# Kernel optimization log

Hardware: AMD Instinct MI355X
Metric: run time of the kernel (lower is better)

The kernel has to match this reference:

```python
import jax, jax.numpy as jnp
import numpy as np

N = 100000   # total nodes across the ragged graph batch
E = 800000   # edges
B = 4096     # graphs
V = 103      # element vocab (embedding rows)
D_IN = 200   # embedding dim
H = 256      # hidden dim


def setup_inputs() -> dict:
    key = jax.random.key(0)
    ks = jax.random.split(key, 20)
    s = 0.05
    return {
        "weight": jax.random.normal(ks[0], (V, D_IN), jnp.float32),
        "sto_x": jax.random.randint(ks[1], (N,), 0, V),
        "sto_edge_index": jax.random.randint(ks[2], (2, E), 0, N),
        "sto_weight": jax.random.uniform(ks[3], (N,), jnp.float32),
        "sto_batch": jnp.sort(jax.random.randint(ks[4], (N,), 0, B)),
        "gW0": jax.random.normal(ks[5], (D_IN, H), jnp.float32) * s,
        "gb0": jnp.zeros((H,), jnp.float32),
        "gW1": jax.random.normal(ks[6], (H, H), jnp.float32) * s,
        "gb1": jnp.zeros((H,), jnp.float32),
        "gW2": jax.random.normal(ks[7], (H, H), jnp.float32) * s,
        "gb2": jnp.zeros((H,), jnp.float32),
        "lstm_Wih": jax.random.normal(ks[8], (4 * H, 2 * H), jnp.float32) * s,
        "lstm_Whh": jax.random.normal(ks[9], (4 * H, H), jnp.float32) * s,
        "lstm_bih": jnp.zeros((4 * H,), jnp.float32),
        "lstm_bhh": jnp.zeros((4 * H,), jnp.float32),
        "mlin_W": jax.random.normal(ks[10], (H, 2 * H), jnp.float32) * s,
        "mlin_b": jnp.zeros((H,), jnp.float32),
        "p0W": jax.random.normal(ks[11], (128, H), jnp.float32) * s,
        "p0b": jnp.zeros((128,), jnp.float32),
        "p1W": jax.random.normal(ks[12], (128, 128), jnp.float32) * s,
        "p1b": jnp.zeros((128,), jnp.float32),
        "p2W": jax.random.normal(ks[13], (1, 128), jnp.float32) * s,
        "p2b": jnp.zeros((1,), jnp.float32),
    }


def reference(weight, sto_x, sto_edge_index, sto_weight, sto_batch,
              gW0, gb0, gW1, gb1, gW2, gb2,
              lstm_Wih, lstm_Whh, lstm_bih, lstm_bhh,
              mlin_W, mlin_b, p0W, p0b, p1W, p1b, p2W, p2b):
    # embedding gather (sto_x - 1, with -1 wrapping to the last row as in torch)
    x = weight[sto_x - 1]

    # --- GCN (3 layers, symmetric norm with self-loops, ReLU between layers) ---
    loop = jnp.arange(N)
    src = jnp.concatenate([sto_edge_index[0], loop])
    dst = jnp.concatenate([sto_edge_index[1], loop])
    deg = jax.ops.segment_sum(jnp.ones_like(dst, jnp.float32), dst, N)
    dinv = jax.lax.rsqrt(jnp.maximum(deg, 1.0))
    norm = (dinv[src] * dinv[dst])[:, None]

    def conv(h_in, W, b):
        hw = h_in @ W                                   # [N, H]
        return jax.ops.segment_sum(hw[src] * norm, dst, N) + b

    x = jax.nn.relu(conv(x, gW0, gb0))
    x = jax.nn.relu(conv(x, gW1, gb1))
    x = conv(x, gW2, gb2)

    # --- stoichiometric weighting + graph-wise scatter sum ---
    wx = x * sto_weight[:, None]                        # [N, H]
    sto = jax.ops.segment_sum(wx, sto_batch, B)         # [B, H]

    # --- Set2Set pooling (2 processing steps, 1-layer LSTM) ---
    h = jnp.zeros((B, H), wx.dtype)
    c = jnp.zeros((B, H), wx.dtype)
    q_star = jnp.zeros((B, 2 * H), wx.dtype)
    for _ in range(2):
        gates = q_star @ lstm_Wih.T + lstm_bih + h @ lstm_Whh.T + lstm_bhh
        i, f, g, o = jnp.split(gates, 4, axis=-1)
        c = jax.nn.sigmoid(f) * c + jax.nn.sigmoid(i) * jnp.tanh(g)
        h = jax.nn.sigmoid(o) * jnp.tanh(c)
        e = jnp.sum(wx * h[sto_batch], axis=-1)         # [N]
        emax = jax.ops.segment_max(e, sto_batch, B)
        a = jnp.exp(e - emax[sto_batch])
        a = a / (jax.ops.segment_sum(a, sto_batch, B)[sto_batch] + 1e-16)
        r = jax.ops.segment_sum(wx * a[:, None], sto_batch, B)
        q_star = jnp.concatenate([h, r], axis=-1)

    mean = q_star @ mlin_W.T + mlin_b + sto
    mean = mean / jnp.maximum(jnp.linalg.norm(mean, axis=1, keepdims=True), 1e-12)

    # --- predictor MLP (LeakyReLU slope 0.01) ---
    y = jax.nn.leaky_relu(mean @ p0W.T + p0b)
    y = jax.nn.leaky_relu(y @ p1W.T + p1b)
    return y @ p2W.T + p2b                              # [B, 1]
```

## Files before the change

kernel.cpp:

```cpp
#include <hip/hip_runtime.h>
#include <math.h>

constexpr int Nn  = 100000;
constexpr int Ee  = 800000;
constexpr int Bb  = 4096;
constexpr int Vv  = 103;
constexpr int DIN = 200;
constexpr int Hh  = 256;
constexpr int KV  = 128;

constexpr int SCHUNK = 1024;
constexpr int NSCAN  = (Nn + SCHUNK - 1)/SCHUNK;

using short8 = __attribute__((ext_vector_type(8))) short;
using f32x4  = __attribute__((ext_vector_type(4))) float;

__device__ __forceinline__ float sigf(float x){ return 1.f/(1.f+expf(-x)); }

__device__ __forceinline__ unsigned short f2bf(float f){
  unsigned int u = __float_as_uint(f);
  u += 0x7FFFu + ((u >> 16) & 1u);
  return (unsigned short)(u >> 16);
}
__device__ __forceinline__ float bf2f(unsigned int u){
  return __uint_as_float((u & 0xFFFFu) << 16);
}

__global__ void k_transpose(const float* __restrict__ in, float* __restrict__ out, int R, int C){
  int idx = blockIdx.x*256 + threadIdx.x;
  if (idx >= R*C) return;
  int r = idx / C, c = idx % C;
  out[(size_t)c*R + r] = in[(size_t)r*C + c];
}

__global__ void k_transpose_b(const float* __restrict__ in, unsigned short* __restrict__ out, int R, int C){
  int idx = blockIdx.x*256 + threadIdx.x;
  if (idx >= R*C) return;
  int r = idx / C, c = idx % C;
  out[(size_t)c*R + r] = f2bf(in[(size_t)r*C + c]);
}

__global__ void k_castb(const float* __restrict__ in, unsigned short* __restrict__ out, int n){
  int i = blockIdx.x*256 + threadIdx.x;
  if (i < n) out[i] = f2bf(in[i]);
}

__global__ void k_wg0t(const float* __restrict__ WG0, unsigned short* __restrict__ WG0tb){
  int i = blockIdx.x*256 + threadIdx.x;
  if (i >= Hh*KV) return;
  int n = i >> 7, k = i & (KV-1);
  float v = (k < Vv) ? WG0[(size_t)k*Hh + n] : 0.f;
  WG0tb[i] = f2bf(v);
}

__global__ void k_packW(const float* __restrict__ Wih, const float* __restrict__ Whh,
                        unsigned short* __restrict__ Wp){
  int i = blockIdx.x*256 + threadIdx.x;
  if (i >= 4*Hh*3*Hh) return;
  int g = i / (3*Hh), j = i % (3*Hh);
  float v = (j < 2*Hh) ? Wih[(size_t)g*2*Hh + j] : Whh[(size_t)g*Hh + (j - 2*Hh)];
  Wp[i] = f2bf(v);
}

__global__ void k_count(const int* __restrict__ dst, int* __restrict__ counts){
  int e = blockIdx.x*256 + threadIdx.x;
  if (e < Ee) atomicAdd(&counts[dst[e]], 1);
}

__global__ void k_dinv(const int* __restrict__ counts, float* __restrict__ dinv){
  int n = blockIdx.x*256 + threadIdx.x;
  if (n < Nn) dinv[n] = rsqrtf((float)(counts[n] + 1));
}

__global__ void k_scan1(const int* __restrict__ counts, int* __restrict__ partial){
  __shared__ int red[256];
  int t = threadIdx.x;
  int base = blockIdx.x*SCHUNK + t*4;
  int s = 0;
  if (base + 3 < Nn){ int4 v = *reinterpret_cast<const int4*>(counts + base); s = v.x+v.y+v.z+v.w; }
  else { for (int i=0;i<4;++i) if (base+i<Nn) s += counts[base+i]; }
  red[t] = s; __syncthreads();
  for (int st=128; st>0; st>>=1){ if (t<st) red[t]+=red[t+st]; __syncthreads(); }
  if (t==0) partial[blockIdx.x] = red[0];
}

__global__ void k_scan2(int* __restrict__ partial, int n){
  __shared__ int buf[128];
  int t = threadIdx.x;
  int v = (t < n) ? partial[t] : 0;
  buf[t] = v; __syncthreads();
  for (int off=1; off<128; off<<=1){
    int tv = (t>=off) ? buf[t-off] : 0;
    __syncthreads();
    buf[t] += tv;
    __syncthreads();
  }
  if (t < n) partial[t] = buf[t] - v;
}

__global__ void k_scan3(const int* __restrict__ counts, const int* __restrict__ partial,
                        int* __restrict__ offs){
  __shared__ int red[256];
  int t = threadIdx.x;
  int base = blockIdx.x*SCHUNK + t*4;
  int c0=0,c1=0,c2=0,c3=0;
  if (base + 3 < Nn){ int4 v = *reinterpret_cast<const int4*>(counts + base); c0=v.x;c1=v.y;c2=v.z;c3=v.w; }
  else { if (base<Nn) c0=counts[base]; if (base+1<Nn) c1=counts[base+1];
         if (base+2<Nn) c2=counts[base+2]; if (base+3<Nn) c3=counts[base+3]; }
  int s = c0+c1+c2+c3;
  red[t] = s; __syncthreads();
  for (int off=1; off<256; off<<=1){
    int tv = (t>=off) ? red[t-off] : 0;
    __syncthreads();
    red[t] += tv;
    __syncthreads();
  }
  int run = partial[blockIdx.x] + red[t] - s;
  if (base   < Nn) offs[base]   = run; run += c0;
  if (base+1 < Nn) offs[base+1] = run; run += c1;
  if (base+2 < Nn) offs[base+2] = run; run += c2;
  if (base+3 < Nn) offs[base+3] = run; run += c3;
  if (blockIdx.x == gridDim.x-1 && t == 255) offs[Nn] = partial[blockIdx.x] + red[255];
}

__global__ void k_copyi(const int* __restrict__ a, int* __restrict__ b, int n){
  int i = blockIdx.x*256 + threadIdx.x;
  if (i < n) b[i] = a[i];
}

__global__ void k_fill(const int* __restrict__ ei, const float* __restrict__ dinv,
                       int* __restrict__ fptr, uint2* __restrict__ epack){
  int e = blockIdx.x*256 + threadIdx.x;
  if (e >= Ee) return;
  int s = ei[e], d = ei[Ee + e];
  int pos = atomicAdd(&fptr[d], 1);
  epack[pos] = make_uint2((unsigned int)s, __float_as_uint(dinv[s]*dinv[d]));
}

__global__ void k_boffs(const int* __restrict__ batch, int* __restrict__ boffs){
  int b = blockIdx.x*256 + threadIdx.x;
  if (b > Bb) return;
  int lo = 0, hi = Nn;
  while (lo < hi){ int mid = (lo+hi)>>1; if (batch[mid] < b) lo = mid+1; else hi = mid; }
  boffs[b] = lo;
}

__global__ void k_hist(const int* __restrict__ sto_x, const int* __restrict__ offs,
                       const uint2* __restrict__ epack, const float* __restrict__ dinv,
                       unsigned short* __restrict__ Vb){
  __shared__ float hist[4][KV];
  int wid = threadIdx.x >> 6, lane = threadIdx.x & 63;
  int n = blockIdx.x*4 + wid;
  hist[wid][lane] = 0.f; hist[wid][lane+64] = 0.f;
  __syncthreads();
  int s = offs[n], e = offs[n+1];
  for (int k = s + lane; k < e; k += 64){
    uint2 ev = epack[k];
    int r2 = sto_x[ev.x]; r2 = (r2 == 0) ? (Vv-1) : r2-1;
    atomicAdd(&hist[wid][r2], __uint_as_float(ev.y));
  }
  if (lane == 0){
    int r0 = sto_x[n]; r0 = (r0 == 0) ? (Vv-1) : r0-1;
    float dn = dinv[n];
    atomicAdd(&hist[wid][r0], dn*dn);
  }
  __syncthreads();
  unsigned int p = ((unsigned int)f2bf(hist[wid][2*lane+1]) << 16) | f2bf(hist[wid][2*lane]);
  ((unsigned int*)Vb)[(size_t)n*(KV/2) + lane] = p;
}

__global__ void k_agg(const unsigned short* __restrict__ Xb, const int* __restrict__ offs,
                      const uint2* __restrict__ epack, const float* __restrict__ dinv,
                      unsigned short* __restrict__ T){
  int wid = threadIdx.x >> 6, lane = threadIdx.x & 63;
  int n = blockIdx.x*4 + wid;
  const uint2* Xv = (const uint2*)Xb;
  uint2 v = Xv[(size_t)n*64 + lane];
  float dn = dinv[n]; float s2 = dn*dn;
  float a0 = bf2f(v.x)*s2, a1 = bf2f(v.x>>16)*s2;
  float a2 = bf2f(v.y)*s2, a3 = bf2f(v.y>>16)*s2;
  int s = offs[n], e = offs[n+1];
  int k = s;
  for (; k + 7 < e; k += 8){
    uint2 ev[8], g[8];
    #pragma unroll
    for (int j = 0; j < 8; ++j) ev[j] = epack[k+j];
    #pragma unroll
    for (int j = 0; j < 8; ++j) g[j] = Xv[(size_t)ev[j].x*64 + lane];
    #pragma unroll
    for (int j = 0; j < 8; ++j){
      float nn = __uint_as_float(ev[j].y);
      a0 += bf2f(g[j].x)*nn; a1 += bf2f(g[j].x>>16)*nn;
      a2 += bf2f(g[j].y)*nn; a3 += bf2f(g[j].y>>16)*nn;
    }
  }
  for (; k + 1 < e; k += 2){
    uint2 e0 = epack[k], e1 = epack[k+1];
    uint2 g0 = Xv[(size_t)e0.x*64 + lane];
    uint2 g1 = Xv[(size_t)e1.x*64 + lane];
    float n0 = __uint_as_float(e0.y), n1 = __uint_as_float(e1.y);
    a0 += bf2f(g0.x)*n0; a1 += bf2f(g0.x>>16)*n0; a2 += bf2f(g0.y)*n0; a3 += bf2f(g0.y>>16)*n0;
    a0 += bf2f(g1.x)*n1; a1 += bf2f(g1.x>>16)*n1; a2 += bf2f(g1.y)*n1; a3 += bf2f(g1.y>>16)*n1;
  }
  if (k < e){
    uint2 e0 = epack[k];
    uint2 g0 = Xv[(size_t)e0.x*64 + lane];
    float n0 = __uint_as_float(e0.y);
    a0 += bf2f(g0.x)*n0; a1 += bf2f(g0.x>>16)*n0;
    a2 += bf2f(g0.y)*n0; a3 += bf2f(g0.y>>16)*n0;
  }
  uint2 o;
  o.x = (unsigned int)f2bf(a0) | ((unsigned int)f2bf(a1) << 16);
  o.y = (unsigned int)f2bf(a2) | ((unsigned int)f2bf(a3) << 16);
  ((uint2*)T)[(size_t)n*64 + lane] = o;
}

__global__ __launch_bounds__(512) void k_gemm64(
    const unsigned short* __restrict__ A, int lda,
    const unsigned short* __restrict__ Bt,
    const float* __restrict__ bias, const float* __restrict__ rowscale,
    const float* __restrict__ addf,
    float* __restrict__ Cf, unsigned short* __restrict__ Cb,
    int M, int K, int Nc, int relu)
{
  __shared__ unsigned short lds[23040];
  unsigned short (*Al)[72] = (unsigned short(*)[72])lds;
  unsigned short (*Bl)[72] = (unsigned short(*)[72])(lds + 64*72);

  int tid = threadIdx.x;
  int w = tid >> 6, lane = tid & 63;
  int wr = (w >> 2)*32, wc = (w & 3)*64;
  int l16 = lane & 15, kh = lane >> 4;
  int rbase = blockIdx.y*64, cbase = blockIdx.x*256;
  int sr = tid >> 3, sb = tid & 7;

  f32x4 acc[2][4] = {};

  for (int k0 = 0; k0 < K; k0 += 64){
    int kk = k0 + sb*8;
    uint4 a0 = make_uint4(0,0,0,0);
    int ar = rbase + sr;
    if (ar < M) a0 = *reinterpret_cast<const uint4*>(A + (size_t)ar*lda + kk);
    uint4 b0 = *reinterpret_cast<const uint4*>(Bt + (size_t)(cbase + sr      )*K + kk);
    uint4 b1 = *reinterpret_cast<const uint4*>(Bt + (size_t)(cbase + sr +  64)*K + kk);
    uint4 b2 = *reinterpret_cast<const uint4*>(Bt + (size_t)(cbase + sr + 128)*K + kk);
    uint4 b3 = *reinterpret_cast<const uint4*>(Bt + (size_t)(cbase + sr + 192)*K + kk);
    __syncthreads();
    *reinterpret_cast<uint4*>(&Al[sr][sb*8])     = a0;
    *reinterpret_cast<uint4*>(&Bl[sr][sb*8])     = b0;
    *reinterpret_cast<uint4*>(&Bl[sr+64][sb*8])  = b1;
    *reinterpret_cast<uint4*>(&Bl[sr+128][sb*8]) = b2;
    *reinterpret_cast<uint4*>(&Bl[sr+192][sb*8]) = b3;
    __syncthreads();

    #pragma unroll
    for (int kq = 0; kq < 2; ++kq){
      short8 af[2], bfv[4];
      #pragma unroll
      for (int m = 0; m < 2; ++m)
        af[m] = *reinterpret_cast<const short8*>(&Al[wr + m*16 + l16][kq*32 + kh*8]);
      #pragma unroll
      for (int n2 = 0; n2 < 4; ++n2)
        bfv[n2] = *reinterpret_cast<const short8*>(&Bl[wc + n2*16 + l16][kq*32 + kh*8]);
      #pragma unroll
      for (int m = 0; m < 2; ++m)
        #pragma unroll
        for (int n2 = 0; n2 < 4; ++n2)
          acc[m][n2] = __builtin_amdgcn_mfma_f32_16x16x32_bf16(af[m], bfv[n2], acc[m][n2], 0, 0, 0);
    }
  }

  if (Cf){
    #pragma unroll
    for (int n2 = 0; n2 < 4; ++n2){
      int col = cbase + wc + n2*16 + l16;
      float bv = bias ? bias[col] : 0.f;
      #pragma unroll
      for (int m = 0; m < 2; ++m){
        #pragma unroll
        for (int i = 0; i < 4; ++i){
          int row = rbase + wr + m*16 + kh*4 + i;
          if (row >= M) continue;
          float v = acc[m][n2][i] + bv;
          if (addf) v += addf[(size_t)row*Nc + col];
          if (rowscale) v *= rowscale[row];
          if (relu == 1) v = fmaxf(v, 0.f);
          else if (relu == 2) v = (v > 0.f) ? v : 0.01f*v;
          Cf[(size_t)row*Nc + col] = v;
        }
      }
    }
  }
  if (Cb){
    __syncthreads();
    unsigned short* eps = lds + w*(32*72);
    #pragma unroll
    for (int n2 = 0; n2 < 4; ++n2){
      int colg = cbase + wc + n2*16 + l16;
      float bv = bias ? bias[colg] : 0.f;
      #pragma unroll
      for (int m = 0; m < 2; ++m){
        #pragma unroll
        for (int i = 0; i < 4; ++i){
          int lrow = m*16 + kh*4 + i;
          int rowg = rbase + wr + lrow;
          float v = acc[m][n2][i] + bv;
          float rs = (rowscale && rowg < M) ? rowscale[rowg] : 1.f;
          v *= rs;
          if (relu == 1) v = fmaxf(v, 0.f);
          else if (relu == 2) v = (v > 0.f) ? v : 0.01f*v;
          eps[lrow*72 + n2*16 + l16] = f2bf(v);
        }
      }
    }
    int c8 = lane & 7;
    #pragma unroll
    for (int rd = 0; rd < 4; ++rd){
      int lrow = rd*8 + (lane >> 3);
      int rowg = rbase + wr + lrow;
      short8 vv = *reinterpret_cast<const short8*>(&eps[lrow*72 + c8*8]);
      if (rowg < M)
        *reinterpret_cast<short8*>(Cb + (size_t)rowg*Nc + cbase + wc + c8*8) = vv;
    }
  }
}

__global__ __launch_bounds__(512) void k_gemm8(
    const unsigned short* __restrict__ A, int lda,
    const unsigned short* __restrict__ Bt,
    const float* __restrict__ bias, const float* __restrict__ rowscale,
    const float* __restrict__ addf,
    float* __restrict__ Cf, unsigned short* __restrict__ Cb,
    int M, int K, int Nc, int relu)
{
  __shared__ unsigned short lds[18432];
  unsigned short (*Al)[40] = (unsigned short(*)[40])lds;
  unsigned short (*Bl)[40] = (unsigned short(*)[40])(lds + 128*40);

  int tid = threadIdx.x;
  int w = tid >> 6, lane = tid & 63;
  int wr = (w >> 1)*32, wc = (w & 1)*64;
  int l16 = lane & 15, kh = lane >> 4;
  int rbase = blockIdx.y*128, cbase = blockIdx.x*128;
  int sr = tid >> 2, sb = tid & 3;

  f32x4 acc[2][4] = {};

  for (int k0 = 0; k0 < K; k0 += 32){
    int kk = k0 + sb*8;
    uint4 a0 = make_uint4(0,0,0,0);
    int ar0 = rbase + sr;
    if (ar0 < M) a0 = *reinterpret_cast<const uint4*>(A + (size_t)ar0*lda + kk);
    uint4 b0 = *reinterpret_cast<const uint4*>(Bt + (size_t)(cbase + sr)*K + kk);
    __syncthreads();
    *reinterpret_cast<uint4*>(&Al[sr][sb*8]) = a0;
    *reinterpret_cast<uint4*>(&Bl[sr][sb*8]) = b0;
    __syncthreads();

    short8 af[2], bfv[4];
    #pragma unroll
    for (int m = 0; m < 2; ++m) af[m] = *reinterpret_cast<const short8*>(&Al[wr + m*16 + l16][kh*8]);
    #pragma unroll
    for (int n2 = 0; n2 < 4; ++n2) bfv[n2] = *reinterpret_cast<const short8*>(&Bl[wc + n2*16 + l16][kh*8]);
    #pragma unroll
    for (int m = 0; m < 2; ++m)
      #pragma unroll
      for (int n2 = 0; n2 < 4; ++n2)
        acc[m][n2] = __builtin_amdgcn_mfma_f32_16x16x32_bf16(af[m], bfv[n2], acc[m][n2], 0, 0, 0);
  }

  if (Cf){
    #pragma unroll
    for (int n2 = 0; n2 < 4; ++n2){
      int col = cbase + wc + n2*16 + l16;
      float bv = bias ? bias[col] : 0.f;
      #pragma unroll
      for (int m = 0; m < 2; ++m){
        #pragma unroll
        for (int i = 0; i < 4; ++i){
          int row = rbase + wr + m*16 + kh*4 + i;
          if (row >= M) continue;
          float v = acc[m][n2][i] + bv;
          if (addf) v += addf[(size_t)row*Nc + col];
          if (rowscale) v *= rowscale[row];
          if (relu == 1) v = fmaxf(v, 0.f);
          else if (relu == 2) v = (v > 0.f) ? v : 0.01f*v;
          Cf[(size_t)row*Nc + col] = v;
        }
      }
    }
  }
  if (Cb){
    __syncthreads();
    unsigned short* eps = lds + w*(32*72);
    #pragma unroll
    for (int n2 = 0; n2 < 4; ++n2){
      int colg = cbase + wc + n2*16 + l16;
      float bv = bias ? bias[colg] : 0.f;
      #pragma unroll
      for (int m = 0; m < 2; ++m){
        #pragma unroll
        for (int i = 0; i < 4; ++i){
          int lrow = m*16 + kh*4 + i;
          int rowg = rbase + wr + lrow;
          float v = acc[m][n2][i] + bv;
          float rs = (rowscale && rowg < M) ? rowscale[rowg] : 1.f;
          v *= rs;
          if (relu == 1) v = fmaxf(v, 0.f);
          else if (relu == 2) v = (v > 0.f) ? v : 0.01f*v;
          eps[lrow*72 + n2*16 + l16] = f2bf(v);
        }
      }
    }
    int c8 = lane & 7;
    #pragma unroll
    for (int rd = 0; rd < 4; ++rd){
      int lrow = rd*8 + (lane >> 3);
      int rowg = rbase + wr + lrow;
      short8 vv = *reinterpret_cast<const short8*>(&eps[lrow*72 + c8*8]);
      if (rowg < M)
        *reinterpret_cast<short8*>(Cb + (size_t)rowg*Nc + cbase + wc + c8*8) = vv;
    }
  }
}

__global__ __launch_bounds__(256) void k_gemm_nt(
    const float* __restrict__ A, const float* __restrict__ Bt,
    const float* __restrict__ bias, const float* __restrict__ Dadd,
    float* __restrict__ C, int M, int K, int Nc, int accum, int act)
{
  __shared__ float As[64][20];
  __shared__ float Bs[64][20];
  int tid = threadIdx.x;
  int rbase = blockIdx.y*64, cbase = blockIdx.x*64;
  int ty = tid>>4, tx = tid&15;
  int lr = tid>>2, lq = tid&3;
  float acc[4][4] = {};
  for (int k0 = 0; k0 < K; k0 += 16){
    float4 av = make_float4(0,0,0,0), bv = make_float4(0,0,0,0);
    int kk = k0 + lq*4;
    int ar = rbase + lr;
    if (ar < M && kk < K){
      if (kk + 3 < K) av = *reinterpret_cast<const float4*>(A + (size_t)ar*K + kk);
      else { float t0[4] = {0,0,0,0}; for (int i=0; i<4 && kk+i<K; ++i) t0[i] = A[(size_t)ar*K + kk + i];
             av = make_float4(t0[0],t0[1],t0[2],t0[3]); }
    }
    int br = cbase + lr;
    if (br < Nc && kk < K){
      if (kk + 3 < K) bv = *reinterpret_cast<const float4*>(Bt + (size_t)br*K + kk);
      else { float t0[4] = {0,0,0,0}; for (int i=0; i<4 && kk+i<K; ++i) t0[i] = Bt[(size_t)br*K + kk + i];
             bv = make_float4(t0[0],t0[1],t0[2],t0[3]); }
    }
    __syncthreads();
    *reinterpret_cast<float4*>(&As[lr][lq*4]) = av;
    *reinterpret_cast<float4*>(&Bs[lr][lq*4]) = bv;
    __syncthreads();
    #pragma unroll
    for (int kc = 0; kc < 16; kc += 4){
      float4 a4[4], b4[4];
      #pragma unroll
      for (int i=0;i<4;++i) a4[i] = *reinterpret_cast<float4*>(&As[ty*4+i][kc]);
      #pragma unroll
      for (int j=0;j<4;++j) b4[j] = *reinterpret_cast<float4*>(&Bs[tx*4+j][kc]);
      #pragma unroll
      for (int i=0;i<4;++i)
        #pragma unroll
        for (int j=0;j<4;++j)
          acc[i][j] += a4[i].x*b4[j].x + a4[i].y*b4[j].y + a4[i].z*b4[j].z + a4[i].w*b4[j].w;
    }
  }
  #pragma unroll
  for (int i=0;i<4;++i){
    int r = rbase + ty*4 + i;
    if (r >= M) continue;
    #pragma unroll
    for (int j=0;j<4;++j){
      int cc = cbase + tx*4 + j;
      if (cc >= Nc) continue;
      float v = acc[i][j];
      if (accum) v += C[(size_t)r*Nc + cc];
      if (bias)  v += bias[cc];
      if (Dadd)  v += Dadd[(size_t)r*Nc + cc];
      if (act == 1) v = (v > 0.f) ? v : 0.01f*v;
      C[(size_t)r*Nc + cc] = v;
    }
  }
}

__global__ void k_bsum(const float* __restrict__ bih, const float* __restrict__ bhh,
                       float* __restrict__ bsum){
  int g = blockIdx.x*256 + threadIdx.x;
  if (g < 4*Hh) bsum[g] = bih[g] + bhh[g];
}

__global__ void k_lstm(const float* __restrict__ gates, float* __restrict__ cbuf,
                       float* __restrict__ hbuf, unsigned short* __restrict__ qh){
  int idx = blockIdx.x*256 + threadIdx.x;
  if (idx >= Bb*Hh) return;
  int b = idx >> 8, ch = idx & 255;
  const float* g = gates + (size_t)b*4*Hh;
  float ig = sigf(g[ch]);
  float fg = sigf(g[Hh + ch]);
  float gg = tanhf(g[2*Hh + ch]);
  float og = sigf(g[3*Hh + ch]);
  float cn = fg*cbuf[idx] + ig*gg;
  float hn = og*tanhf(cn);
  cbuf[idx] = cn; hbuf[idx] = hn;
  unsigned short hb = f2bf(hn);
  qh[(size_t)b*3*Hh + ch] = hb;
  qh[(size_t)b*3*Hh + 2*Hh + ch] = hb;
}

__global__ void k_pool(const unsigned short* __restrict__ wxb,
                       const float* __restrict__ hbuf,
                       const int* __restrict__ boffs,
                       unsigned short* __restrict__ qh,
                       float* __restrict__ sto, int do_sto){
  int wid = threadIdx.x >> 6, lane = threadIdx.x & 63;
  int g = blockIdx.x*4 + wid;
  if (g >= Bb) return;
  const uint2* Xv = (const uint2*)wxb;
  float4 hv = ((const float4*)hbuf)[(size_t)g*64 + lane];
  int s = boffs[g], e = boffs[g+1];
  float m = -INFINITY, ssum = 0.f;
  float a0=0.f,a1=0.f,a2=0.f,a3=0.f;
  float t0=0.f,t1=0.f,t2=0.f,t3=0.f;
  for (int n = s; n < e; ++n){
    uint2 v = Xv[(size_t)n*64 + lane];
    float x0=bf2f(v.x), x1=bf2f(v.x>>16), x2=bf2f(v.y), x3=bf2f(v.y>>16);
    if (do_sto){ t0+=x0; t1+=x1; t2+=x2; t3+=x3; }
    float d = x0*hv.x + x1*hv.y + x2*hv.z + x3*hv.w;
    #pragma unroll
    for (int mask=32; mask; mask>>=1) d += __shfl_xor(d, mask, 64);
    if (d > m){
      float sc = expf(m - d);
      ssum = ssum*sc + 1.f;
      a0 = a0*sc + x0; a1 = a1*sc + x1; a2 = a2*sc + x2; a3 = a3*sc + x3;
      m = d;
    } else {
      float p = expf(d - m);
      ssum += p;
      a0 += p*x0; a1 += p*x1; a2 += p*x2; a3 += p*x3;
    }
  }
  float inv = 1.f/(ssum + 1e-16f);
  uint2 o;
  o.x = (unsigned int)f2bf(a0*inv) | ((unsigned int)f2bf(a1*inv) << 16);
  o.y = (unsigned int)f2bf(a2*inv) | ((unsigned int)f2bf(a3*inv) << 16);
  ((uint2*)(qh + (size_t)g*3*Hh + Hh))[lane] = o;
  if (do_sto) ((float4*)sto)[(size_t)g*64 + lane] = make_float4(t0,t1,t2,t3);
}

__global__ void k_norm(float* __restrict__ mean, unsigned short* __restrict__ outb){
  __shared__ float red[256];
  int b = blockIdx.x, tid = threadIdx.x;
  float v = mean[(size_t)b*Hh + tid];
  red[tid] = v*v; __syncthreads();
  for (int st=128; st>0; st>>=1){ if (tid<st) red[tid] += red[tid+st]; __syncthreads(); }
  float nrm = fmaxf(sqrtf(red[0]), 1e-12f);
  float o = v/nrm;
  outb[(size_t)b*Hh + tid] = f2bf(o);
}

__global__ void k_out(const float* __restrict__ y1, const float* __restrict__ p2W,
                      const float* __restrict__ p2b, float* __restrict__ out){
  __shared__ float red[128];
  int b = blockIdx.x, tid = threadIdx.x;
  float v = y1[(size_t)b*128 + tid]*p2W[tid];
  red[tid] = v; __syncthreads();
  for (int st=64; st>0; st>>=1){ if (tid<st) red[tid] += red[tid+st]; __syncthreads(); }
  if (tid == 0) out[b] = red[0] + p2b[0];
}

extern "C" void kernel_launch(void* const* d_in, const int* in_sizes, int n_in,
                              void* d_out, int out_size, void* d_ws, size_t ws_size,
                              hipStream_t stream) {
  const float* weight   = (const float*)d_in[0];
  const int*   sto_x    = (const int*)  d_in[1];
  const int*   ei       = (const int*)  d_in[2];
  const float* sto_w    = (const float*)d_in[3];
  const int*   batch    = (const int*)  d_in[4];
  const float* gW0 = (const float*)d_in[5];   const float* gb0 = (const float*)d_in[6];
  const float* gW1 = (const float*)d_in[7];   const float* gb1 = (const float*)d_in[8];
  const float* gW2 = (const float*)d_in[9];   const float* gb2 = (const float*)d_in[10];
  const float* Wih = (const float*)d_in[11];  const float* Whh = (const float*)d_in[12];
  const float* bih = (const float*)d_in[13];  const float* bhh = (const float*)d_in[14];
  const float* mW  = (const float*)d_in[15];  const float* mb  = (const float*)d_in[16];
  const float* p0W = (const float*)d_in[17];  const float* p0b = (const float*)d_in[18];
  const float* p1W = (const float*)d_in[19];  const float* p1b = (const float*)d_in[20];
  const float* p2W = (const float*)d_in[21];  const float* p2b = (const float*)d_in[22];
  float* out = (float*)d_out;

  char* w = (char*)d_ws;
  auto alloc = [&](size_t bytes)->char*{ char* p = w; w += (bytes + 255) & ~size_t(255); return p; };
  unsigned short* Xb = (unsigned short*)alloc((size_t)Nn*Hh*2);
  unsigned short* Tb = (unsigned short*)alloc((size_t)Nn*Hh*2);
  unsigned short* Vb = (unsigned short*)alloc((size_t)Nn*KV*2);
  float* WG0   = (float*)alloc((size_t)Vv*Hh*4);
  unsigned short* WG0tb = (unsigned short*)alloc((size_t)Hh*KV*2);
  float* gW0t  = (float*)alloc((size_t)Hh*DIN*4);
  unsigned short* gW1tb = (unsigned short*)alloc((size_t)Hh*Hh*2);
  unsigned short* gW2tb = (unsigned short*)alloc((size_t)Hh*Hh*2);
  unsigned short* Wpb   = (unsigned short*)alloc((size_t)4*Hh*3*Hh*2);
  unsigned short* mWb   = (unsigned short*)alloc((size_t)Hh*2*Hh*2);
  unsigned short* p0Wb  = (unsigned short*)alloc((size_t)128*Hh*2);
  unsigned short* p1Wb  = (unsigned short*)alloc((size_t)128*128*2);
  int*   counts= (int*)  alloc((size_t)Nn*4);
  int*   offs  = (int*)  alloc((size_t)(Nn+1)*4);
  int*   fptr  = (int*)  alloc((size_t)Nn*4);
  int*   spart = (int*)  alloc((size_t)NSCAN*4);
  float* dinv  = (float*)alloc((size_t)Nn*4);
  uint2* epack = (uint2*)alloc((size_t)Ee*8);
  int*   boffs = (int*)  alloc((size_t)(Bb+1)*4);
  float* sto   = (float*)alloc((size_t)Bb*Hh*4);
  float* hbuf  = (float*)alloc((size_t)Bb*Hh*4);
  float* cbuf  = (float*)alloc((size_t)Bb*Hh*4);
  unsigned short* qh = (unsigned short*)alloc((size_t)Bb*3*Hh*2);
  float* gates = (float*)alloc((size_t)Bb*4*Hh*4);
  float* bsum  = (float*)alloc((size_t)4*Hh*4);
  float* meanb = (float*)alloc((size_t)Bb*Hh*4);
  unsigned short* meanbb = (unsigned short*)alloc((size_t)Bb*Hh*2);
  unsigned short* y0b = (unsigned short*)alloc((size_t)Bb*128*2);
  float* y1    = (float*)alloc((size_t)Bb*128*4);

  auto gemm = [&](const float* A, const float* Bt, const float* bias, const float* Dadd,
                  float* C, int M, int K, int Nc, int accum, int act){
    dim3 g((Nc+63)/64, (M+63)/64);
    k_gemm_nt<<<g, 256, 0, stream>>>(A, Bt, bias, Dadd, C, M, K, Nc, accum, act);
  };
  auto gemm8 = [&](const unsigned short* A, int lda, const unsigned short* Bt,
                   const float* bias, const float* rowscale, const float* addf,
                   float* Cf, unsigned short* Cb, int M, int K, int Nc, int relu){
    dim3 g(Nc/128, (M+127)/128);
    k_gemm8<<<g, 512, 0, stream>>>(A, lda, Bt, bias, rowscale, addf, Cf, Cb, M, K, Nc, relu);
  };
  auto gemm64 = [&](const unsigned short* A, int lda, const unsigned short* Bt,
                    const float* bias, const float* rowscale, const float* addf,
                    float* Cf, unsigned short* Cb, int M, int K, int Nc, int relu){
    dim3 g(Nc/256, (M+63)/64);
    k_gemm64<<<g, 512, 0, stream>>>(A, lda, Bt, bias, rowscale, addf, Cf, Cb, M, K, Nc, relu);
  };

  hipMemsetAsync(counts, 0, (size_t)Nn*4, stream);
  hipMemsetAsync(cbuf,  0, (size_t)Bb*Hh*4, stream);
  hipMemsetAsync(qh,    0, (size_t)Bb*3*Hh*2, stream);

  k_transpose<<<(DIN*Hh+255)/256, 256, 0, stream>>>(gW0, gW0t, DIN, Hh);
  k_transpose_b<<<(Hh*Hh+255)/256, 256, 0, stream>>>(gW1, gW1tb, Hh, Hh);
  k_transpose_b<<<(Hh*Hh+255)/256, 256, 0, stream>>>(gW2, gW2tb, Hh, Hh);
  k_packW<<<(4*Hh*3*Hh+255)/256, 256, 0, stream>>>(Wih, Whh, Wpb);
  k_castb<<<(Hh*2*Hh+255)/256, 256, 0, stream>>>(mW, mWb, Hh*2*Hh);
  k_castb<<<(128*Hh+255)/256, 256, 0, stream>>>(p0W, p0Wb, 128*Hh);
  k_castb<<<(128*128+255)/256, 256, 0, stream>>>(p1W, p1Wb, 128*128);

  k_count<<<(Ee+255)/256, 256, 0, stream>>>(ei + Ee, counts);
  k_dinv<<<(Nn+255)/256, 256, 0, stream>>>(counts, dinv);
  k_scan1<<<NSCAN, 256, 0, stream>>>(counts, spart);
  k_scan2<<<1, 128, 0, stream>>>(spart, NSCAN);
  k_scan3<<<NSCAN, 256, 0, stream>>>(counts, spart, offs);
  k_copyi<<<(Nn+255)/256, 256, 0, stream>>>(offs, fptr, Nn);
  k_fill<<<(Ee+255)/256, 256, 0, stream>>>(ei, dinv, fptr, epack);
  k_boffs<<<(Bb+256)/256, 256, 0, stream>>>(batch, boffs);

  gemm(weight, gW0t, nullptr, nullptr, WG0, Vv, DIN, Hh, 0, 0);
  k_wg0t<<<(Hh*KV+255)/256, 256, 0, stream>>>(WG0, WG0tb);
  k_hist<<<Nn/4, 256, 0, stream>>>(sto_x, offs, epack, dinv, Vb);
  gemm64(Vb, KV, WG0tb, gb0, nullptr, nullptr, nullptr, Xb, Nn, KV, Hh, 1);

  k_agg<<<Nn/4, 256, 0, stream>>>(Xb, offs, epack, dinv, Tb);
  gemm64(Tb, Hh, gW1tb, gb1, nullptr, nullptr, nullptr, Xb, Nn, Hh, Hh, 1);
  k_agg<<<Nn/4, 256, 0, stream>>>(Xb, offs, epack, dinv, Tb);
  gemm64(Tb, Hh, gW2tb, gb2, sto_w, nullptr, nullptr, Xb, Nn, Hh, Hh, 0);

  k_bsum<<<(4*Hh+255)/256, 256, 0, stream>>>(bih, bhh, bsum);

  for (int t = 0; t < 2; ++t){
    gemm64(qh, 3*Hh, Wpb, bsum, nullptr, nullptr, gates, nullptr, Bb, 3*Hh, 4*Hh, 0);
    k_lstm<<<(Bb*Hh+255)/256, 256, 0, stream>>>(gates, cbuf, hbuf, qh);
    k_pool<<<Bb/4, 256, 0, stream>>>(Xb, hbuf, boffs, qh, sto, t == 0);
  }

  gemm64(qh, 3*Hh, mWb, mb, nullptr, sto, meanb, nullptr, Bb, 2*Hh, Hh, 0);
  k_norm<<<Bb, Hh, 0, stream>>>(meanb, meanbb);
  gemm8(meanbb, Hh, p0Wb, p0b, nullptr, nullptr, nullptr, y0b, Bb, Hh, 128, 2);
  gemm8(y0b, 128, p1Wb, p1b, nullptr, nullptr, y1, nullptr, Bb, 128, 128, 2);
  k_out<<<Bb, 128, 0, stream>>>(y1, p2W, p2b, out);
}
```

Before: 560.3 us.

## Replace histogram+GEMM first GCN layer with direct gather of projected embeddings

The first GCN layer previously built a per-node 128-bin vocabulary histogram and then ran a dense N×128×256 GEMM. It now gathers bf16 rows of the precomputed weight@W0 table per edge (using a per-edge byte vocab index written during CSR fill) and applies bias and ReLU directly. Separately, many small prep kernels (transposes, casts, batch offsets, bias sum, dinv, copy) are merged into one prep kernel or folded into the scan kernels to cut launch count. The trade is more gather traffic per edge in exchange for removing the histogram atomics, the intermediate Vb buffer and one large GEMM.

Result: no change. 551.0 us (-1.7%).

```diff
diff --git a/kernel.cpp b/kernel.cpp
--- a/kernel.cpp
+++ b/kernel.cpp
@@ -7,7 +7,6 @@
 constexpr int Vv  = 103;
 constexpr int DIN = 200;
 constexpr int Hh  = 256;
-constexpr int KV  = 128;
 
 constexpr int SCHUNK = 1024;
 constexpr int NSCAN  = (Nn + SCHUNK - 1)/SCHUNK;
@@ -26,40 +25,70 @@
   return __uint_as_float((u & 0xFFFFu) << 16);
 }
 
-__global__ void k_transpose(const float* __restrict__ in, float* __restrict__ out, int R, int C){
+constexpr int PW_A = DIN*Hh;
+constexpr int PW_B = Hh*Hh;
+constexpr int PW_C = Hh*Hh;
+constexpr int PW_D = 4*Hh*3*Hh;
+constexpr int PW_E = Hh*2*Hh;
+constexpr int PW_F = 128*Hh;
+constexpr int PW_G = 128*128;
+constexpr int PW_H = Bb + 1;
+constexpr int PW_I = 4*Hh;
+constexpr int PW_TOT = PW_A+PW_B+PW_C+PW_D+PW_E+PW_F+PW_G+PW_H+PW_I;
+
+__global__ void k_prep(const float* __restrict__ gW0, float* __restrict__ gW0t,
+                       const float* __restrict__ gW1, unsigned short* __restrict__ gW1tb,
+                       const float* __restrict__ gW2, unsigned short* __restrict__ gW2tb,
+                       const float* __restrict__ Wih, const float* __restrict__ Whh,
+                       unsigned short* __restrict__ Wpb,
+                       const float* __restrict__ mW, unsigned short* __restrict__ mWb,
+                       const float* __restrict__ p0W, unsigned short* __restrict__ p0Wb,
+                       const float* __restrict__ p1W, unsigned short* __restrict__ p1Wb,
+                       const int* __restrict__ batch, int* __restrict__ boffs,
+                       const float* __restrict__ bih, const float* __restrict__ bhh,
+                       float* __restrict__ bsum){
   int idx = blockIdx.x*256 + threadIdx.x;
-  if (idx >= R*C) return;
-  int r = idx / C, c = idx % C;
-  out[(size_t)c*R + r] = in[(size_t)r*C + c];
-}
-
-__global__ void k_transpose_b(const float* __restrict__ in, unsigned short* __restrict__ out, int R, int C){
-  int idx = blockIdx.x*256 + threadIdx.x;
-  if (idx >= R*C) return;
-  int r = idx / C, c = idx % C;
-  out[(size_t)c*R + r] = f2bf(in[(size_t)r*C + c]);
-}
-
-__global__ void k_castb(const float* __restrict__ in, unsigned short* __restrict__ out, int n){
-  int i = blockIdx.x*256 + threadIdx.x;
-  if (i < n) out[i] = f2bf(in[i]);
-}
-
-__global__ void k_wg0t(const float* __restrict__ WG0, unsigned short* __restrict__ WG0tb){
-  int i = blockIdx.x*256 + threadIdx.x;
-  if (i >= Hh*KV) return;
-  int n = i >> 7, k = i & (KV-1);
-  float v = (k < Vv) ? WG0[(size_t)k*Hh + n] : 0.f;
-  WG0tb[i] = f2bf(v);
-}
-
-__global__ void k_packW(const float* __restrict__ Wih, const float* __restrict__ Whh,
-                        unsigned short* __restrict__ Wp){
-  int i = blockIdx.x*256 + threadIdx.x;
-  if (i >= 4*Hh*3*Hh) return;
-  int g = i / (3*Hh), j = i % (3*Hh);
-  float v = (j < 2*Hh) ? Wih[(size_t)g*2*Hh + j] : Whh[(size_t)g*Hh + (j - 2*Hh)];
-  Wp[i] = f2bf(v);
+  if (idx >= PW_TOT) return;
+  if (idx < PW_A){
+    int r = idx / Hh, c = idx % Hh;
+    gW0t[(size_t)c*DIN + r] = gW0[idx];
+    return;
+  }
+  idx -= PW_A;
+  if (idx < PW_B){
+    int r = idx >> 8, c = idx & 255;
+    gW1tb[(size_t)c*Hh + r] = f2bf(gW1[idx]);
+    return;
+  }
+  idx -= PW_B;
+  if (idx < PW_C){
+    int r = idx >> 8, c = idx & 255;
+    gW2tb[(size_t)c*Hh + r] = f2bf(gW2[idx]);
+    return;
+  }
+  idx -= PW_C;
+  if (idx < PW_D){
+    int g = idx / (3*Hh), j = idx % (3*Hh);
+    float v = (j < 2*Hh) ? Wih[(size_t)g*2*Hh + j] : Whh[(size_t)g*Hh + (j - 2*Hh)];
+    Wpb[idx] = f2bf(v);
+    return;
+  }
+  idx -= PW_D;
+  if (idx < PW_E){ mWb[idx] = f2bf(mW[idx]); return; }
+  idx -= PW_E;
+  if (idx < PW_F){ p0Wb[idx] = f2bf(p0W[idx]); return; }
+  idx -= PW_F;
+  if (idx < PW_G){ p1Wb[idx] = f2bf(p1W[idx]); return; }
+  idx -= PW_G;
+  if (idx < PW_H){
+    int b = idx;
+    int lo = 0, hi = Nn;
+    while (lo < hi){ int mid = (lo+hi)>>1; if (batch[mid] < b) lo = mid+1; else hi = mid; }
+    boffs[b] = lo;
+    return;
+  }
+  idx -= PW_H;
+  bsum[idx] = bih[idx] + bhh[idx];
 }
 
 __global__ void k_count(const int* __restrict__ dst, int* __restrict__ counts){
@@ -67,18 +96,22 @@
   if (e < Ee) atomicAdd(&counts[dst[e]], 1);
 }
 
-__global__ void k_dinv(const int* __restrict__ counts, float* __restrict__ dinv){
-  int n = blockIdx.x*256 + threadIdx.x;
-  if (n < Nn) dinv[n] = rsqrtf((float)(counts[n] + 1));
-}
-
-__global__ void k_scan1(const int* __restrict__ counts, int* __restrict__ partial){
+__global__ void k_scan1(const int* __restrict__ counts, int* __restrict__ partial,
+                        float* __restrict__ dinv){
   __shared__ int red[256];
   int t = threadIdx.x;
   int base = blockIdx.x*SCHUNK + t*4;
   int s = 0;
-  if (base + 3 < Nn){ int4 v = *reinterpret_cast<const int4*>(counts + base); s = v.x+v.y+v.z+v.w; }
-  else { for (int i=0;i<4;++i) if (base+i<Nn) s += counts[base+i]; }
+  if (base + 3 < Nn){
+    int4 v = *reinterpret_cast<const int4*>(counts + base);
+    s = v.x+v.y+v.z+v.w;
+    dinv[base]   = rsqrtf((float)(v.x + 1));
+    dinv[base+1] = rsqrtf((float)(v.y + 1));
+    dinv[base+2] = rsqrtf((float)(v.z + 1));
+    dinv[base+3] = rsqrtf((float)(v.w + 1));
+  } else {
+    for (int i=0;i<4;++i) if (base+i<Nn){ int c = counts[base+i]; s += c; dinv[base+i] = rsqrtf((float)(c+1)); }
+  }
   red[t] = s; __syncthreads();
   for (int st=128; st>0; st>>=1){ if (t<st) red[t]+=red[t+st]; __syncthreads(); }
   if (t==0) partial[blockIdx.x] = red[0];
@@ -99,7 +132,7 @@
 }
 
 __global__ void k_scan3(const int* __restrict__ counts, const int* __restrict__ partial,
-                        int* __restrict__ offs){
+                        int* __restrict__ offs, int* __restrict__ fptr){
   __shared__ int red[256];
   int t = threadIdx.x;
   int base = blockIdx.x*SCHUNK + t*4;
@@ -116,57 +149,66 @@
     __syncthreads();
   }
   int run = partial[blockIdx.x] + red[t] - s;
-  if (base   < Nn) offs[base]   = run; run += c0;
-  if (base+1 < Nn) offs[base+1] = run; run += c1;
-  if (base+2 < Nn) offs[base+2] = run; run += c2;
-  if (base+3 < Nn) offs[base+3] = run; run += c3;
+  if (base   < Nn){ offs[base]   = run; fptr[base]   = run; } run += c0;
+  if (base+1 < Nn){ offs[base+1] = run; fptr[base+1] = run; } run += c1;
+  if (base+2 < Nn){ offs[base+2] = run; fptr[base+2] = run; } run += c2;
+  if (base+3 < Nn){ offs[base+3] = run; fptr[base+3] = run; } run += c3;
   if (blockIdx.x == gridDim.x-1 && t == 255) offs[Nn] = partial[blockIdx.x] + red[255];
 }
 
-__global__ void k_copyi(const int* __restrict__ a, int* __restrict__ b, int n){
-  int i = blockIdx.x*256 + threadIdx.x;
-  if (i < n) b[i] = a[i];
-}
-
 __global__ void k_fill(const int* __restrict__ ei, const float* __restrict__ dinv,
-                       int* __restrict__ fptr, uint2* __restrict__ epack){
+                       const int* __restrict__ sto_x, int* __restrict__ fptr,
+                       uint2* __restrict__ epack, unsigned char* __restrict__ evoc){
   int e = blockIdx.x*256 + threadIdx.x;
   if (e >= Ee) return;
   int s = ei[e], d = ei[Ee + e];
   int pos = atomicAdd(&fptr[d], 1);
   epack[pos] = make_uint2((unsigned int)s, __float_as_uint(dinv[s]*dinv[d]));
-}
-
-__global__ void k_boffs(const int* __restrict__ batch, int* __restrict__ boffs){
-  int b = blockIdx.x*256 + threadIdx.x;
-  if (b > Bb) return;
-  int lo = 0, hi = Nn;
-  while (lo < hi){ int mid = (lo+hi)>>1; if (batch[mid] < b) lo = mid+1; else hi = mid; }
-  boffs[b] = lo;
-}
-
-__global__ void k_hist(const int* __restrict__ sto_x, const int* __restrict__ offs,
-                       const uint2* __restrict__ epack, const float* __restrict__ dinv,
-                       unsigned short* __restrict__ Vb){
-  __shared__ float hist[4][KV];
+  int v = sto_x[s];
+  evoc[pos] = (unsigned char)((v == 0) ? (Vv-1) : v-1);
+}
+
+__global__ void k_conv0(const unsigned short* __restrict__ WG0b, const int* __restrict__ sto_x,
+                        const int* __restrict__ offs, const uint2* __restrict__ epack,
+                        const unsigned char* __restrict__ evoc, const float* __restrict__ dinv,
+                        const float* __restrict__ bias, unsigned short* __restrict__ Xb){
   int wid = threadIdx.x >> 6, lane = threadIdx.x & 63;
   int n = blockIdx.x*4 + wid;
-  hist[wid][lane] = 0.f; hist[wid][lane+64] = 0.f;
-  __syncthreads();
+  const uint2* Wv = (const uint2*)WG0b;
+  int v0 = sto_x[n]; int r0 = (v0 == 0) ? (Vv-1) : v0-1;
+  float dn = dinv[n]; float s2 = dn*dn;
+  uint2 w0 = Wv[(size_t)r0*64 + lane];
+  float a0 = bf2f(w0.x)*s2, a1 = bf2f(w0.x>>16)*s2;
+  float a2 = bf2f(w0.y)*s2, a3 = bf2f(w0.y>>16)*s2;
   int s = offs[n], e = offs[n+1];
-  for (int k = s + lane; k < e; k += 64){
+  int k = s;
+  for (; k + 7 < e; k += 8){
+    uint2 ev[8]; int rv[8]; uint2 g[8];
+    #pragma unroll
+    for (int j = 0; j < 8; ++j){ ev[j] = epack[k+j]; rv[j] = evoc[k+j]; }
+    #pragma unroll
+    for (int j = 0; j < 8; ++j) g[j] = Wv[(size_t)rv[j]*64 + lane];
+    #pragma unroll
+    for (int j = 0; j < 8; ++j){
+      float nn = __uint_as_float(ev[j].y);
+      a0 += bf2f(g[j].x)*nn; a1 += bf2f(g[j].x>>16)*nn;
+      a2 += bf2f(g[j].y)*nn; a3 += bf2f(g[j].y>>16)*nn;
+    }
+  }
+  for (; k < e; ++k){
     uint2 ev = epack[k];
-    int r2 = sto_x[ev.x]; r2 = (r2 == 0) ? (Vv-1) : r2-1;
-    atomicAdd(&hist[wid][r2], __uint_as_float(ev.y));
-  }
-  if (lane == 0){
-    int r0 = sto_x[n]; r0 = (r0 == 0) ? (Vv-1) : r0-1;
-    float dn = dinv[n];
-    atomicAdd(&hist[wid][r0], dn*dn);
-  }
-  __syncthreads();
-  unsigned int p = ((unsigned int)f2bf(hist[wid][2*lane+1]) << 16) | f2bf(hist[wid][2*lane]);
-  ((unsigned int*)Vb)[(size_t)n*(KV/2) + lane] = p;
+    uint2 g = Wv[(size_t)evoc[k]*64 + lane];
+    float nn = __uint_as_float(ev.y);
+    a0 += bf2f(g.x)*nn; a1 += bf2f(g.x>>16)*nn;
+    a2 += bf2f(g.y)*nn; a3 += bf2f(g.y>>16)*nn;
+  }
+  float4 bv = ((const float4*)bias)[lane];
+  a0 = fmaxf(a0 + bv.x, 0.f); a1 = fmaxf(a1 + bv.y, 0.f);
+  a2 = fmaxf(a2 + bv.z, 0.f); a3 = fmaxf(a3 + bv.w, 0.f);
+  uint2 o;
+  o.x = (unsigned int)f2bf(a0) | ((unsigned int)f2bf(a1) << 16);
+  o.y = (unsigned int)f2bf(a2) | ((unsigned int)f2bf(a3) << 16);
+  ((uint2*)Xb)[(size_t)n*64 + lane] = o;
 }
 
 __global__ void k_agg(const unsigned short* __restrict__ Xb, const int* __restrict__ offs,
@@ -426,8 +468,8 @@
 
 __global__ __launch_bounds__(256) void k_gemm_nt(
     const float* __restrict__ A, const float* __restrict__ Bt,
-    const float* __restrict__ bias, const float* __restrict__ Dadd,
-    float* __restrict__ C, int M, int K, int Nc, int accum, int act)
+    float* __restrict__ C, unsigned short* __restrict__ Cb,
+    int M, int K, int Nc)
 {
   __shared__ float As[64][20];
   __shared__ float Bs[64][20];
@@ -478,19 +520,10 @@
       int cc = cbase + tx*4 + j;
       if (cc >= Nc) continue;
       float v = acc[i][j];
-      if (accum) v += C[(size_t)r*Nc + cc];
-      if (bias)  v += bias[cc];
-      if (Dadd)  v += Dadd[(size_t)r*Nc + cc];
-      if (act == 1) v = (v > 0.f) ? v : 0.01f*v;
-      C[(size_t)r*Nc + cc] = v;
-    }
-  }
-}
-
-__global__ void k_bsum(const float* __restrict__ bih, const float* __restrict__ bhh,
-                       float* __restrict__ bsum){
-  int g = blockIdx.x*256 + threadIdx.x;
-  if (g < 4*Hh) bsum[g] = bih[g] + bhh[g];
+      if (C)  C[(size_t)r*Nc + cc] = v;
+      if (Cb) Cb[(size_t)r*Nc + cc] = f2bf(v);
+    }
+  }
 }
 
 __global__ void k_lstm(const float* __restrict__ gates, float* __restrict__ cbuf,
@@ -595,9 +628,8 @@
   auto alloc = [&](size_t bytes)->char*{ char* p = w; w += (bytes + 255) & ~size_t(255); return p; };
   unsigned short* Xb = (unsigned short*)alloc((size_t)Nn*Hh*2);
   unsigned short* Tb = (unsigned short*)alloc((size_t)Nn*Hh*2);
-  unsigned short* Vb = (unsigned short*)alloc((size_t)Nn*KV*2);
   float* WG0   = (float*)alloc((size_t)Vv*Hh*4);
-  unsigned short* WG0tb = (unsigned short*)alloc((size_t)Hh*KV*2);
+  unsigned short* WG0b = (unsigned short*)alloc((size_t)Vv*Hh*2);
   float* gW0t  = (float*)alloc((size_t)Hh*DIN*4);
   unsigned short* gW1tb = (unsigned short*)alloc((size_t)Hh*Hh*2);
   unsigned short* gW2tb = (unsigned short*)alloc((size_t)Hh*Hh*2);
@@ -611,6 +643,7 @@
   int*   spart = (int*)  alloc((size_t)NSCAN*4);
   float* dinv  = (float*)alloc((size_t)Nn*4);
   uint2* epack = (uint2*)alloc((size_t)Ee*8);
+  unsigned char* evoc = (unsigned char*)alloc((size_t)Ee);
   int*   boffs = (int*)  alloc((size_t)(Bb+1)*4);
   float* sto   = (float*)alloc((size_t)Bb*Hh*4);
   float* hbuf  = (float*)alloc((size_t)Bb*Hh*4);
@@ -623,11 +656,6 @@
   unsigned short* y0b = (unsigned short*)alloc((size_t)Bb*128*2);
   float* y1    = (float*)alloc((size_t)Bb*128*4);
 
-  auto gemm = [&](const float* A, const float* Bt, const float* bias, const float* Dadd,
-                  float* C, int M, int K, int Nc, int accum, int act){
-    dim3 g((Nc+63)/64, (M+63)/64);
-    k_gemm_nt<<<g, 256, 0, stream>>>(A, Bt, bias, Dadd, C, M, K, Nc, accum, act);
-  };
   auto gemm8 = [&](const unsigned short* A, int lda, const unsigned short* Bt,
                    const float* bias, const float* rowscale, const float* addf,
                    float* Cf, unsigned short* Cb, int M, int K, int Nc, int relu){
@@ -645,34 +673,26 @@
   hipMemsetAsync(cbuf,  0, (size_t)Bb*Hh*4, stream);
   hipMemsetAsync(qh,    0, (size_t)Bb*3*Hh*2, stream);
 
-  k_transpose<<<(DIN*Hh+255)/256, 256, 0, stream>>>(gW0, gW0t, DIN, Hh);
-  k_transpose_b<<<(Hh*Hh+255)/256, 256, 0, stream>>>(gW1, gW1tb, Hh, Hh);
-  k_transpose_b<<<(Hh*Hh+255)/256, 256, 0, stream>>>(gW2, gW2tb, Hh, Hh);
-  k_packW<<<(4*Hh*3*Hh+255)/256, 256, 0, stream>>>(Wih, Whh, Wpb);
-  k_castb<<<(Hh*2*Hh+255)/256, 256, 0, stream>>>(mW, mWb, Hh*2*Hh);
-  k_castb<<<(128*Hh+255)/256, 256, 0, stream>>>(p0W, p0Wb, 128*Hh);
-  k_castb<<<(128*128+255)/256, 256, 0, stream>>>(p1W, p1Wb, 128*128);
+  k_prep<<<(PW_TOT+255)/256, 256, 0, stream>>>(
+      gW0, gW0t, gW1, gW1tb, gW2, gW2tb, Wih, Whh, Wpb,
+      mW, mWb, p0W, p0Wb, p1W, p1Wb, batch, boffs, bih, bhh, bsum);
 
   k_count<<<(Ee+255)/256, 256, 0, stream>>>(ei + Ee, counts);
-  k_dinv<<<(Nn+255)/256, 256, 0, stream>>>(counts, dinv);
-  k_scan1<<<NSCAN, 256, 0, stream>>>(counts, spart);
+  k_scan1<<<NSCAN, 256, 0, stream>>>(counts, spart, dinv);
   k_scan2<<<1, 128, 0, stream>>>(spart, NSCAN);
-  k_scan3<<<NSCAN, 256, 0, stream>>>(counts, spart, offs);
-  k_copyi<<<(Nn+255)/256, 256, 0, stream>>>(offs, fptr, Nn);
-  k_fill<<<(Ee+255)/256, 256, 0, stream>>>(ei, dinv, fptr, epack);
-  k_boffs<<<(Bb+256)/256, 256, 0, stream>>>(batch, boffs);
-
-  gemm(weight, gW0t, nullptr, nullptr, WG0, Vv, DIN, Hh, 0, 0);
-  k_wg0t<<<(Hh*KV+255)/256, 256, 0, stream>>>(WG0, WG0tb);
-  k_hist<<<Nn/4, 256, 0, stream>>>(sto_x, offs, epack, dinv, Vb);
-  gemm64(Vb, KV, WG0tb, gb0, nullptr, nullptr, nullptr, Xb, Nn, KV, Hh, 1);
+  k_scan3<<<NSCAN, 256, 0, stream>>>(counts, spart, offs, fptr);
+  k_fill<<<(Ee+255)/256, 256, 0, stream>>>(ei, dinv, sto_x, fptr, epack, evoc);
+
+  {
+    dim3 g((Hh+63)/64, (Vv+63)/64);
+    k_gemm_nt<<<g, 256, 0, stream>>>(weight, gW0t, WG0, WG0b, Vv, DIN, Hh);
+  }
+  k_conv0<<<Nn/4, 256, 0, stream>>>(WG0b, sto_x, offs, epack, evoc, dinv, gb0, Xb);
 
   k_agg<<<Nn/4, 256, 0, stream>>>(Xb, offs, epack, dinv, Tb);
   gemm64(Tb, Hh, gW1tb, gb1, nullptr, nullptr, nullptr, Xb, Nn, Hh, Hh, 1);
   k_agg<<<Nn/4, 256, 0, stream>>>(Xb, offs, epack, dinv, Tb);
   gemm64(Tb, Hh, gW2tb, gb2, sto_w, nullptr, nullptr, Xb, Nn, Hh, Hh, 0);
-
-  k_bsum<<<(4*Hh+255)/256, 256, 0, stream>>>(bih, bhh, bsum);
 
   for (int t = 0; t < 2; ++t){
     gemm64(qh, 3*Hh, Wpb, bsum, nullptr, nullptr, gates, nullptr, Bb, 3*Hh, 4*Hh, 0);
```
